# Performance work log

Hardware: AMD Instinct MI355X
Metric: run time of the kernel (lower is better)

Reference implementation:

```python
import jax, jax.numpy as jnp
import numpy as np

D_MODEL = 1024
N_HEADS = 16
D_K = D_MODEL // N_HEADS
THETA = 10000.0
MAX_SEQ_LEN = 2048


def _rope_tables(seq_len):
    pos = jnp.arange(seq_len, dtype=jnp.float32)
    inv_freq = 1.0 / (THETA ** (jnp.arange(0, D_K, 2, dtype=jnp.float32) / D_K))
    ang = pos[:, None] * inv_freq[None, :]  # [T, D_K/2]
    return jnp.cos(ang), jnp.sin(ang)


def _apply_rope(x, cos, sin):
    # x: [..., T, D_K]; cos/sin: [T, D_K/2]
    x_even = x[..., ::2]
    x_odd = x[..., 1::2]
    r_even = x_even * cos - x_odd * sin
    r_odd = x_even * sin + x_odd * cos
    out = jnp.stack([r_even, r_odd], axis=-1)  # [..., T, D_K/2, 2]
    return out.reshape(x.shape)


def setup_inputs() -> dict:
    key = jax.random.key(0)
    ks = jax.random.split(key, 5)
    std = np.sqrt(2.0 / (D_MODEL + D_MODEL))
    x = jax.random.normal(ks[0], (2, 2048, D_MODEL), dtype=jnp.float32)
    w_q = jax.random.normal(ks[1], (D_MODEL, D_MODEL), dtype=jnp.float32) * std
    w_k = jax.random.normal(ks[2], (D_MODEL, D_MODEL), dtype=jnp.float32) * std
    w_v = jax.random.normal(ks[3], (D_MODEL, D_MODEL), dtype=jnp.float32) * std
    w_o = jax.random.normal(ks[4], (D_MODEL, D_MODEL), dtype=jnp.float32) * std
    return {"x": x, "w_q": w_q, "w_k": w_k, "w_v": w_v, "w_o": w_o}


def reference(x, w_q, w_k, w_v, w_o):
    B, T, _ = x.shape
    # projections: weight stored as [d_out, d_in], y = x @ W^T
    q = jnp.einsum('btd,od->bto', x, w_q)
    k = jnp.einsum('btd,od->bto', x, w_k)
    v = jnp.einsum('btd,od->bto', x, w_v)
    # split heads: [B, T, H*Dk] -> [B, H, T, Dk]
    q = q.reshape(B, T, N_HEADS, D_K).transpose(0, 2, 1, 3)
    k = k.reshape(B, T, N_HEADS, D_K).transpose(0, 2, 1, 3)
    v = v.reshape(B, T, N_HEADS, D_K).transpose(0, 2, 1, 3)
    cos, sin = _rope_tables(T)
    q = _apply_rope(q, cos, sin)
    k = _apply_rope(k, cos, sin)
    scores = jnp.einsum('bhqd,bhkd->bhqk', q, k) / np.sqrt(D_K).astype(np.float32)
    causal = jnp.tril(jnp.ones((T, T), dtype=bool))
    scores = jnp.where(causal, scores, -jnp.inf)
    attn = jax.nn.softmax(scores, axis=-1)
    out = jnp.einsum('bhqk,bhkd->bhqd', attn, v)
    out = out.transpose(0, 2, 1, 3).reshape(B, T, D_MODEL)
    return jnp.einsum('btd,od->bto', out, w_o)
```

## Files before the change

### kernel.cpp

```cpp
#include <hip/hip_runtime.h>
#include <hip/hip_bf16.h>

typedef __bf16 bf16_t;
typedef __bf16 bf16x8 __attribute__((ext_vector_type(8)));
typedef float f32x4 __attribute__((ext_vector_type(4)));
typedef short short4v __attribute__((ext_vector_type(4)));
typedef unsigned int uint2v __attribute__((ext_vector_type(2)));

#define D_MODEL 1024
#define T_SEQ 2048
#define NH 16
#define DKD 64
#define X_ELEMS (4194304u)
#define W_ELEMS (1048576u)
#define Q_SCALE 0.18033688011112042f

__device__ __forceinline__ void async16(const bf16_t* g, bf16_t* l) {
    __builtin_amdgcn_global_load_lds((const __attribute__((address_space(1))) void*)g,
                                     (__attribute__((address_space(3))) void*)l, 16, 0, 0);
}

__device__ __forceinline__ unsigned ldsa(const bf16_t* p) {
    return (unsigned)(size_t)(const __attribute__((address_space(3))) bf16_t*)p;
}

__global__ __launch_bounds__(256) void convert_kernel(
    const float* __restrict__ x, const float* __restrict__ wq,
    const float* __restrict__ wk, const float* __restrict__ wv,
    const float* __restrict__ wo,
    bf16_t* __restrict__ xb, bf16_t* __restrict__ wqb, bf16_t* __restrict__ wkb,
    bf16_t* __restrict__ wvb, bf16_t* __restrict__ wob)
{
    size_t idx = ((size_t)blockIdx.x * 256 + threadIdx.x) * 4;
    const float* src; bf16_t* dst; size_t off;
    if (idx < X_ELEMS) { src = x; dst = xb; off = idx; }
    else {
        size_t r = idx - X_ELEMS;
        unsigned w = (unsigned)(r >> 20);
        off = r & (W_ELEMS - 1);
        src = (w == 0) ? wq : (w == 1) ? wk : (w == 2) ? wv : wo;
        dst = (w == 0) ? wqb : (w == 1) ? wkb : (w == 2) ? wvb : wob;
    }
    float4 v = *(const float4*)(src + off);
    union { bf16_t b[4]; short4v s; } u;
    u.b[0] = (bf16_t)v.x; u.b[1] = (bf16_t)v.y;
    u.b[2] = (bf16_t)v.z; u.b[3] = (bf16_t)v.w;
    *(short4v*)(dst + off) = u.s;
}

__global__ __launch_bounds__(256) void rope_kernel(float* __restrict__ cost, float* __restrict__ sint)
{
    int idx = blockIdx.x * 256 + threadIdx.x;
    int t = idx >> 5, i = idx & 31;
    float inv = expf(-0.28782313662425572f * (float)i);
    float ang = (float)t * inv;
    float s, c;
    sincosf(ang, &s, &c);
    cost[idx] = c; sint[idx] = s;
}

__global__ __launch_bounds__(256) void gemm_fused(
    const bf16_t* __restrict__ A,
    const bf16_t* __restrict__ W0, const bf16_t* __restrict__ W1, const bf16_t* __restrict__ W2,
    bf16_t* __restrict__ qout, bf16_t* __restrict__ kout, bf16_t* __restrict__ vout,
    const float* __restrict__ cost, const float* __restrict__ sint,
    float* __restrict__ fout, int modeBase)
{
    const int K = 1024;
    __shared__ bf16_t As[128 * 32];
    __shared__ bf16_t Bs[128 * 32];
    const int tid = threadIdx.x;
    const int wave = tid >> 6, lane = tid & 63;
    const int quad = lane >> 4, l16 = lane & 15;
    const int m0 = blockIdx.x * 128;
    const int n0 = blockIdx.y * 128;
    const int wm = (wave >> 1) * 64, wn = (wave & 1) * 64;
    const int mode = modeBase + blockIdx.z;
    const bf16_t* W = (mode == 1) ? W1 : (mode == 2) ? W2 : W0;

    const bf16_t* Afrag = (mode == 2) ? Bs : As;
    const bf16_t* Bfrag = (mode == 2) ? As : Bs;
    const int aoff = (mode == 2) ? wn : wm;
    const int boff = (mode == 2) ? wm : wn;

    const f32x4 fzero = {0.f, 0.f, 0.f, 0.f};
    f32x4 acc[4][4];
    #pragma unroll
    for (int i = 0; i < 4; ++i)
        #pragma unroll
        for (int j = 0; j < 4; ++j) acc[i][j] = fzero;

    for (int k0 = 0; k0 < K; k0 += 32) {
        __syncthreads();
        #pragma unroll
        for (int c = 0; c < 2; ++c) {
            int G = c * 256 + tid;
            int row = G >> 2, go = G & 3;
            async16(A + (size_t)(m0 + row) * K + (k0 + go * 8), As + (size_t)(c * 256 + wave * 64) * 8);
            async16(W + (size_t)(n0 + row) * K + (k0 + go * 8), Bs + (size_t)(c * 256 + wave * 64) * 8);
        }
        __syncthreads();
        bf16x8 af[4], bfv[4];
        #pragma unroll
        for (int mi = 0; mi < 4; ++mi)
            af[mi] = *(const bf16x8*)(Afrag + (aoff + mi * 16 + l16) * 32 + quad * 8);
        #pragma unroll
        for (int ni = 0; ni < 4; ++ni)
            bfv[ni] = *(const bf16x8*)(Bfrag + (boff + ni * 16 + l16) * 32 + quad * 8);
        #pragma unroll
        for (int mi = 0; mi < 4; ++mi)
            #pragma unroll
            for (int ni = 0; ni < 4; ++ni)
                acc[mi][ni] = __builtin_amdgcn_mfma_f32_16x16x32_bf16(af[mi], bfv[ni], acc[mi][ni], 0, 0, 0);
    }

    #pragma unroll
    for (int mi = 0; mi < 4; ++mi) {
        #pragma unroll
        for (int ni = 0; ni < 4; ++ni) {
            #pragma unroll
            for (int reg = 0; reg < 4; ++reg) {
                float v = acc[mi][ni][reg];
                if (mode == 2) {
                    int f   = n0 + wn + mi * 16 + quad * 4 + reg;
                    int tok = m0 + wm + ni * 16 + l16;
                    int t = tok & (T_SEQ - 1), b = tok >> 11;
                    int h = f >> 6, dk = f & 63;
                    vout[(((size_t)b * NH + h) * DKD + dk) * T_SEQ + t] = (bf16_t)v;
                } else {
                    int row = m0 + wm + mi * 16 + quad * 4 + reg;
                    int col = n0 + wn + ni * 16 + l16;
                    if (mode == 3) {
                        fout[(size_t)row * D_MODEL + col] = v;
                    } else {
                        int t = row & (T_SEQ - 1), b = row >> 11;
                        int h = col >> 6, dk = col & 63;
                        float vp = __shfl_xor(v, 1);
                        int fi = dk >> 1;
                        float c = cost[t * 32 + fi], s = sint[t * 32 + fi];
                        float r = (dk & 1) ? (vp * s + v * c) : (v * c - vp * s);
                        if (mode == 0) r *= Q_SCALE;
                        bf16_t* dst = (mode == 0) ? qout : kout;
                        dst[(((size_t)b * NH + h) * T_SEQ + t) * DKD + dk] = (bf16_t)r;
                    }
                }
            }
        }
    }
}

__global__ __launch_bounds__(256, 4) void attn_kernel(
    const bf16_t* __restrict__ Q, const bf16_t* __restrict__ Kb,
    const bf16_t* __restrict__ Vt, bf16_t* __restrict__ O,
    float* __restrict__ Opart, float* __restrict__ Lpart)
{
    __shared__ bf16_t Vs[2][4096];
    __shared__ bf16_t Ks[2][4096];
    const int tid = threadIdx.x;
    const int w = tid >> 6;
    const int lane = tid & 63;
    const int quad = lane >> 4, l16 = lane & 15;
    const int sig = ((quad & 1) << 1) | (quad >> 1);
    const int m7 = l16 & 15 & 7;
    const int bh = blockIdx.x;

    int v = 39 - (int)blockIdx.y;
    int g = 0, po = 0;
    for (;; ++g) {
        const int C = (g + 4) >> 2;
        if (v < C) break;
        v -= C;
        if (g >= 4) po += C;
    }
    const int c = v;
    const int ktlo = 8 * c;
    const int kthi = min(8 * c + 8, 2 * g + 2);
    const int qw = (4 * g + w) * 32;

    const bf16_t* kbase = Kb + (size_t)bh * T_SEQ * DKD;
    const bf16_t* vbase = Vt + (size_t)bh * DKD * T_SEQ;

    const int srow = tid >> 3;
    const int sgr  = (tid & 7) ^ (srow & 7);
    const bf16_t* vsrc = vbase + (size_t)srow * T_SEQ + sgr * 8;
    const bf16_t* ksrc = kbase + (size_t)srow * DKD + sgr * 8;

    const unsigned o0  = (unsigned)((l16 * 64 + ((sig ^ m7) * 8)) << 1);
    const unsigned o1  = (unsigned)((l16 * 64 + (((sig + 4) ^ m7) * 8)) << 1);
    const unsigned ko0 = (unsigned)((l16 * 64 + ((quad ^ m7) * 8)) << 1);
    const unsigned ko1 = (unsigned)((l16 * 64 + (((quad + 4) ^ m7) * 8)) << 1);
    const unsigned vb0 = ldsa(Vs[0]), vb1 = ldsa(Vs[1]);
    const unsigned kb0 = ldsa(Ks[0]), kb1 = ldsa(Ks[1]);

    bf16x8 qf[2][2];
    #pragma unroll
    for (int j = 0; j < 2; ++j) {
        const bf16_t* qp = Q + ((size_t)bh * T_SEQ + qw + j * 16 + l16) * DKD;
        qf[j][0] = *(const bf16x8*)(qp + quad * 8);
        qf[j][1] = *(const bf16x8*)(qp + 32 + quad * 8);
    }
    const f32x4 fzero = {0.f, 0.f, 0.f, 0.f};
    f32x4 oacc[2][4];
    #pragma unroll
    for (int j = 0; j < 2; ++j)
        #pragma unroll
        for (int i = 0; i < 4; ++i) oacc[j][i] = fzero;
    float lsum[2] = {0.f, 0.f};

    {
        const bf16_t* vs_ = vsrc + ktlo * 64;
        const bf16_t* ks_ = ksrc + (size_t)ktlo * 64 * DKD;
        async16(vs_,         &Vs[0][0] + w * 512);
        async16(vs_ + 65536, &Vs[0][0] + 2048 + w * 512);
        async16(ks_,         &Ks[0][0] + w * 512);
        async16(ks_ + 2048,  &Ks[0][0] + 2048 + w * 512);
    }
    asm volatile("s_waitcnt vmcnt(0)" ::: "memory");
    __syncthreads();

#define ATT_TILE(VNP, KNP, VCA, KCA) do { \
    const int k0 = kt * 64; \
    if (kt + 1 < kthi) { \
        const bf16_t* vs_ = vsrc + (k0 + 64); \
        const bf16_t* ks_ = ksrc + (size_t)(k0 + 64) * DKD; \
        async16(vs_,         (VNP) + w * 512); \
        async16(vs_ + 65536, (VNP) + 2048 + w * 512); \
        async16(ks_,         (KNP) + w * 512); \
        async16(ks_ + 2048,  (KNP) + 2048 + w * 512); \
    } \
    __builtin_amdgcn_sched_barrier(0); \
    bf16x8 kc00, kc01, kc10, kc11, kc20, kc21, kc30, kc31; \
    { const unsigned kaA = (KCA) + ko0, kaB = (KCA) + ko1; \
      asm volatile( \
        "ds_read_b128 %0, %8 offset:0\n\t" \
        "ds_read_b128 %1, %9 offset:0\n\t" \
        "ds_read_b128 %2, %8 offset:2048\n\t" \
        "ds_read_b128 %3, %9 offset:2048\n\t" \
        "ds_read_b128 %4, %8 offset:4096\n\t" \
        "ds_read_b128 %5, %9 offset:4096\n\t" \
        "ds_read_b128 %6, %8 offset:6144\n\t" \
        "ds_read_b128 %7, %9 offset:6144\n\t" \
        "s_waitcnt lgkmcnt(0)" \
        : "=&v"(kc00), "=&v"(kc01), "=&v"(kc10), "=&v"(kc11), \
          "=&v"(kc20), "=&v"(kc21), "=&v"(kc30), "=&v"(kc31) \
        : "v"(kaA), "v"(kaB)); } \
    __builtin_amdgcn_sched_barrier(0); \
    _Pragma("unroll") \
    for (int j = 0; j < 2; ++j) { \
      if (k0 <= qw + j * 16 + 15) {    \
        const int qcol = qw + j * 16 + l16; \
        f32x4 s[4]; \
        s[0] = __builtin_amdgcn_mfma_f32_16x16x32_bf16(kc00, qf[j][0], fzero, 0, 0, 0); \
        s[0] = __builtin_amdgcn_mfma_f32_16x16x32_bf16(kc01, qf[j][1], s[0], 0, 0, 0); \
        s[1] = __builtin_amdgcn_mfma_f32_16x16x32_bf16(kc10, qf[j][0], fzero, 0, 0, 0); \
        s[1] = __builtin_amdgcn_mfma_f32_16x16x32_bf16(kc11, qf[j][1], s[1], 0, 0, 0); \
        s[2] = __builtin_amdgcn_mfma_f32_16x16x32_bf16(kc20, qf[j][0], fzero, 0, 0, 0); \
        s[2] = __builtin_amdgcn_mfma_f32_16x16x32_bf16(kc21, qf[j][1], s[2], 0, 0, 0); \
        s[3] = __builtin_amdgcn_mfma_f32_16x16x32_bf16(kc30, qf[j][0], fzero, 0, 0, 0); \
        s[3] = __builtin_amdgcn_mfma_f32_16x16x32_bf16(kc31, qf[j][1], s[3], 0, 0, 0); \
        if (k0 + 63 > qw + j * 16) { \
            _Pragma("unroll") \
            for (int fi = 0; fi < 4; ++fi) \
                _Pragma("unroll") \
                for (int reg = 0; reg < 4; ++reg) { \
                    int key = k0 + fi * 16 + quad * 4 + reg; \
                    s[fi][reg] = (key > qcol) ? -__builtin_inff() : s[fi][reg]; \
                } \
        } \
        float sm = 0.f; \
        _Pragma("unroll") \
        for (int fi = 0; fi < 4; ++fi) \
            _Pragma("unroll") \
            for (int reg = 0; reg < 4; ++reg) { \
                float p = __builtin_amdgcn_exp2f(s[fi][reg]); \
                s[fi][reg] = p; sm += p; \
            } \
        lsum[j] += sm; \
        unsigned wv[4][2]; \
        _Pragma("unroll") \
        for (int fi = 0; fi < 4; ++fi) { \
            asm("v_cvt_pk_bf16_f32 %0, %1, %2" : "=v"(wv[fi][0]) : "v"(s[fi][0]), "v"(s[fi][1])); \
            asm("v_cvt_pk_bf16_f32 %0, %1, %2" : "=v"(wv[fi][1]) : "v"(s[fi][2]), "v"(s[fi][3])); \
        } \
        uint2v r0 = __builtin_amdgcn_permlane16_swap(wv[0][0], wv[1][0], false, false); \
        uint2v r1 = __builtin_amdgcn_permlane16_swap(wv[0][1], wv[1][1], false, false); \
        uint2v r2 = __builtin_amdgcn_permlane16_swap(wv[2][0], wv[3][0], false, false); \
        uint2v r3 = __builtin_amdgcn_permlane16_swap(wv[2][1], wv[3][1], false, false); \
        union { unsigned uu[4]; bf16x8 vv; } p0, p1; \
        p0.uu[0] = r0[0]; p0.uu[1] = r1[0]; p0.uu[2] = r0[1]; p0.uu[3] = r1[1]; \
        p1.uu[0] = r2[0]; p1.uu[1] = r3[0]; p1.uu[2] = r2[1]; p1.uu[3] = r3[1]; \
        const unsigned vA = (VCA) + o0, vB = (VCA) + o1; \
        bf16x8 w0a, w0b, w1a, w1b; \
        __builtin_amdgcn_sched_barrier(0); \
        asm volatile( \
            "ds_read_b128 %0, %4 offset:0\n\t" \
            "ds_read_b128 %1, %5 offset:0\n\t" \
            "ds_read_b128 %2, %4 offset:2048\n\t" \
            "ds_read_b128 %3, %5 offset:2048\n\t" \
            "s_waitcnt lgkmcnt(0)" \
            : "=&v"(w0a), "=&v"(w0b), "=&v"(w1a), "=&v"(w1b) \
            : "v"(vA), "v"(vB)); \
        __builtin_amdgcn_sched_barrier(0); \
        oacc[j][0] = __builtin_amdgcn_mfma_f32_16x16x32_bf16(w0a, p0.vv, oacc[j][0], 0, 0, 0); \
        oacc[j][0] = __builtin_amdgcn_mfma_f32_16x16x32_bf16(w0b, p1.vv, oacc[j][0], 0, 0, 0); \
        oacc[j][1] = __builtin_amdgcn_mfma_f32_16x16x32_bf16(w1a, p0.vv, oacc[j][1], 0, 0, 0); \
        oacc[j][1] = __builtin_amdgcn_mfma_f32_16x16x32_bf16(w1b, p1.vv, oacc[j][1], 0, 0, 0); \
        bf16x8 w2a, w2b, w3a, w3b; \
        asm volatile( \
            "ds_read_b128 %0, %4 offset:4096\n\t" \
            "ds_read_b128 %1, %5 offset:4096\n\t" \
            "ds_read_b128 %2, %4 offset:6144\n\t" \
            "ds_read_b128 %3, %5 offset:6144\n\t" \
            "s_waitcnt lgkmcnt(0)" \
            : "=&v"(w2a), "=&v"(w2b), "=&v"(w3a), "=&v"(w3b) \
            : "v"(vA), "v"(vB)); \
        __builtin_amdgcn_sched_barrier(0); \
        oacc[j][2] = __builtin_amdgcn_mfma_f32_16x16x32_bf16(w2a, p0.vv, oacc[j][2], 0, 0, 0); \
        oacc[j][2] = __builtin_amdgcn_mfma_f32_16x16x32_bf16(w2b, p1.vv, oacc[j][2], 0, 0, 0); \
        oacc[j][3] = __builtin_amdgcn_mfma_f32_16x16x32_bf16(w3a, p0.vv, oacc[j][3], 0, 0, 0); \
        oacc[j][3] = __builtin_amdgcn_mfma_f32_16x16x32_bf16(w3b, p1.vv, oacc[j][3], 0, 0, 0); \
      } \
    } \
    asm volatile("s_waitcnt vmcnt(0)" ::: "memory"); \
    __syncthreads(); \
} while (0)

    bool flip = false;
    for (int kt = ktlo; kt < kthi; ++kt) {
        if (!flip) { ATT_TILE(&Vs[1][0], &Ks[1][0], vb0, kb0); }
        else       { ATT_TILE(&Vs[0][0], &Ks[0][0], vb1, kb1); }
        flip = !flip;
    }
#undef ATT_TILE

    if (g < 4) {
        const int b = bh >> 4, h = bh & 15;
        #pragma unroll
        for (int j = 0; j < 2; ++j) {
            float l = lsum[j];
            l += __shfl_xor(l, 16);
            l += __shfl_xor(l, 32);
            float rl = 1.0f / l;
            int q = qw + j * 16 + l16;
            #pragma unroll
            for (int di = 0; di < 4; ++di) {
                union { bf16_t hh[4]; unsigned long long u64; } ok;
                #pragma unroll
                for (int reg = 0; reg < 4; ++reg) ok.hh[reg] = (bf16_t)(oacc[j][di][reg] * rl);
                int d = di * 16 + quad * 4;
                *(unsigned long long*)(O + ((size_t)b * T_SEQ + q) * D_MODEL + h * DKD + d) = ok.u64;
            }
        }
    } else {
        const size_t slot = (size_t)bh * 36 + po + c;
        float* op = Opart + slot * 8192 + (size_t)w * 2048;
        #pragma unroll
        for (int j = 0; j < 2; ++j) {
            Lpart[slot * 512 + w * 128 + j * 64 + lane] = lsum[j];
            #pragma unroll
            for (int di = 0; di < 4; ++di)
                *(f32x4*)(op + ((size_t)(j * 4 + di) * 64 + lane) * 4) = oacc[j][di];
        }
    }
}

__global__ __launch_bounds__(256) void combine_kernel(
    const float* __restrict__ Opart, const float* __restrict__ Lpart, bf16_t* __restrict__ O)
{
    const int bh = blockIdx.x;
    const int g = 4 + blockIdx.y;
    const int C = (g + 4) >> 2;
    int po0 = 0;
    for (int gg = 4; gg < g; ++gg) po0 += (gg + 4) >> 2;
    const int t = threadIdx.x;
    const int ql = t >> 3;
    const int d0 = (t & 7) * 8;
    const int j = ql >> 4, l16 = ql & 15;
    const int di = d0 >> 4;
    const int quad0 = (d0 & 15) >> 2;
    const int b = bh >> 4, h = bh & 15;
    const size_t sb = (size_t)bh * 36 + po0;

    for (int w = 0; w < 4; ++w) {
        float l = 0.f;
        for (int cc = 0; cc < C; ++cc) {
            const float* L = Lpart + (sb + cc) * 512 + w * 128 + j * 64 + l16;
            #pragma unroll
            for (int q = 0; q < 4; ++q) l += L[q * 16];
        }
        const float rl = 1.0f / l;
        union { bf16_t hh[8]; bf16x8 vv; } ov;
        #pragma unroll
        for (int g2 = 0; g2 < 2; ++g2) {
            const int off = ((j * 4 + di) * 64 + (quad0 + g2) * 16 + l16) * 4;
            f32x4 acc = {0.f, 0.f, 0.f, 0.f};
            for (int cc = 0; cc < C; ++cc)
                acc += *(const f32x4*)(Opart + (sb + cc) * 8192 + (size_t)w * 2048 + off);
            #pragma unroll
            for (int reg = 0; reg < 4; ++reg)
                ov.hh[g2 * 4 + reg] = (bf16_t)(acc[reg] * rl);
        }
        const int q = g * 128 + w * 32 + ql;
        *(bf16x8*)(O + ((size_t)b * T_SEQ + q) * D_MODEL + h * DKD + d0) = ov.vv;
    }
}

extern "C" void kernel_launch(void* const* d_in, const int* in_sizes, int n_in,
                              void* d_out, int out_size, void* d_ws, size_t ws_size,
                              hipStream_t stream)
{
    const float* x  = (const float*)d_in[0];
    const float* wq = (const float*)d_in[1];
    const float* wk = (const float*)d_in[2];
    const float* wv = (const float*)d_in[3];
    const float* wo = (const float*)d_in[4];
    float* out = (float*)d_out;

    char* ws = (char*)d_ws;
    size_t off = 0;
    auto alloc = [&](size_t bytes) -> void* {
        void* p = ws + off; off += (bytes + 255) & ~(size_t)255; return p;
    };
    bf16_t* xb   = (bf16_t*)alloc((size_t)X_ELEMS * 2);
    bf16_t* wqb  = (bf16_t*)alloc((size_t)W_ELEMS * 2);
    bf16_t* wkb  = (bf16_t*)alloc((size_t)W_ELEMS * 2);
    bf16_t* wvb  = (bf16_t*)alloc((size_t)W_ELEMS * 2);
    bf16_t* wob  = (bf16_t*)alloc((size_t)W_ELEMS * 2);
    bf16_t* qb   = (bf16_t*)alloc((size_t)X_ELEMS * 2);
    bf16_t* kb   = (bf16_t*)alloc((size_t)X_ELEMS * 2);
    bf16_t* vtb  = (bf16_t*)alloc((size_t)X_ELEMS * 2);
    bf16_t* ob   = (bf16_t*)alloc((size_t)X_ELEMS * 2);
    float*  cost = (float*)alloc((size_t)T_SEQ * 32 * 4);
    float*  sint = (float*)alloc((size_t)T_SEQ * 32 * 4);
    float*  opart = (float*)alloc((size_t)32 * 36 * 8192 * 4);
    float*  lpart = (float*)alloc((size_t)32 * 36 * 512 * 4);

    convert_kernel<<<8192, 256, 0, stream>>>(x, wq, wk, wv, wo, xb, wqb, wkb, wvb, wob);
    rope_kernel<<<256, 256, 0, stream>>>(cost, sint);
    gemm_fused<<<dim3(32, 8, 3), 256, 0, stream>>>(xb, wqb, wkb, wvb, qb, kb, vtb, cost, sint, nullptr, 0);
    attn_kernel<<<dim3(32, 40), 256, 0, stream>>>(qb, kb, vtb, ob, opart, lpart);
    combine_kernel<<<dim3(32, 12), 256, 0, stream>>>(opart, lpart, ob);
    gemm_fused<<<dim3(32, 8, 1), 256, 0, stream>>>(ob, wob, nullptr, nullptr, nullptr, nullptr, nullptr,
                                                   cost, sint, out, 3);
}
```

Baseline: 202.6 us.

## Split-K output projection with atomics and merge rope/zeroing into convert kernel

The output projection GEMM is split along K into two halves across blockIdx.z, and each half accumulates into the fp32 output with atomicAdd. This doubles the block count from 256 to 512 to fill more CUs. The output is zeroed and the rope tables are built inside the convert kernel, which removes one launch. In exchange the output takes an extra 16MB zeroing write, atomic traffic and a nondeterministic summation order.

```diff
diff --git a/kernel.cpp b/kernel.cpp
--- a/kernel.cpp
+++ b/kernel.cpp
@@ -29,34 +29,39 @@
     const float* __restrict__ wk, const float* __restrict__ wv,
     const float* __restrict__ wo,
     bf16_t* __restrict__ xb, bf16_t* __restrict__ wqb, bf16_t* __restrict__ wkb,
-    bf16_t* __restrict__ wvb, bf16_t* __restrict__ wob)
+    bf16_t* __restrict__ wvb, bf16_t* __restrict__ wob,
+    float* __restrict__ cost, float* __restrict__ sint, float* __restrict__ outz)
 {
-    size_t idx = ((size_t)blockIdx.x * 256 + threadIdx.x) * 4;
-    const float* src; bf16_t* dst; size_t off;
-    if (idx < X_ELEMS) { src = x; dst = xb; off = idx; }
-    else {
-        size_t r = idx - X_ELEMS;
-        unsigned w = (unsigned)(r >> 20);
-        off = r & (W_ELEMS - 1);
-        src = (w == 0) ? wq : (w == 1) ? wk : (w == 2) ? wv : wo;
-        dst = (w == 0) ? wqb : (w == 1) ? wkb : (w == 2) ? wvb : wob;
-    }
-    float4 v = *(const float4*)(src + off);
-    union { bf16_t b[4]; short4v s; } u;
-    u.b[0] = (bf16_t)v.x; u.b[1] = (bf16_t)v.y;
-    u.b[2] = (bf16_t)v.z; u.b[3] = (bf16_t)v.w;
-    *(short4v*)(dst + off) = u.s;
-}
-
-__global__ __launch_bounds__(256) void rope_kernel(float* __restrict__ cost, float* __restrict__ sint)
-{
-    int idx = blockIdx.x * 256 + threadIdx.x;
-    int t = idx >> 5, i = idx & 31;
-    float inv = expf(-0.28782313662425572f * (float)i);
-    float ang = (float)t * inv;
-    float s, c;
-    sincosf(ang, &s, &c);
-    cost[idx] = c; sint[idx] = s;
+    const unsigned bid = blockIdx.x;
+    if (bid < 8192) {
+        size_t idx = ((size_t)bid * 256 + threadIdx.x) * 4;
+        const float* src; bf16_t* dst; size_t off;
+        if (idx < X_ELEMS) { src = x; dst = xb; off = idx; }
+        else {
+            size_t r = idx - X_ELEMS;
+            unsigned w = (unsigned)(r >> 20);
+            off = r & (W_ELEMS - 1);
+            src = (w == 0) ? wq : (w == 1) ? wk : (w == 2) ? wv : wo;
+            dst = (w == 0) ? wqb : (w == 1) ? wkb : (w == 2) ? wvb : wob;
+        }
+        float4 v = *(const float4*)(src + off);
+        union { bf16_t b[4]; short4v s; } u;
+        u.b[0] = (bf16_t)v.x; u.b[1] = (bf16_t)v.y;
+        u.b[2] = (bf16_t)v.z; u.b[3] = (bf16_t)v.w;
+        *(short4v*)(dst + off) = u.s;
+    } else if (bid < 8448) {
+        int idx = (int)(bid - 8192) * 256 + threadIdx.x;
+        int t = idx >> 5, i = idx & 31;
+        float inv = expf(-0.28782313662425572f * (float)i);
+        float ang = (float)t * inv;
+        float s, c;
+        sincosf(ang, &s, &c);
+        cost[idx] = c; sint[idx] = s;
+    } else {
+        size_t idx = ((size_t)(bid - 8448) * 256 + threadIdx.x) * 4;
+        float4 z = {0.f, 0.f, 0.f, 0.f};
+        *(float4*)(outz + idx) = z;
+    }
 }
 
 __global__ __launch_bounds__(256) void gemm_fused(
@@ -83,6 +88,9 @@
     const int aoff = (mode == 2) ? wn : wm;
     const int boff = (mode == 2) ? wm : wn;
 
+    const int kLo = (mode >= 3) ? (mode - 3) * 512 : 0;
+    const int kHi = (mode >= 3) ? kLo + 512 : K;
+
     const f32x4 fzero = {0.f, 0.f, 0.f, 0.f};
     f32x4 acc[4][4];
     #pragma unroll
@@ -90,7 +98,7 @@
         #pragma unroll
         for (int j = 0; j < 4; ++j) acc[i][j] = fzero;
 
-    for (int k0 = 0; k0 < K; k0 += 32) {
+    for (int k0 = kLo; k0 < kHi; k0 += 32) {
         __syncthreads();
         #pragma unroll
         for (int c = 0; c < 2; ++c) {
@@ -130,8 +138,8 @@
                 } else {
                     int row = m0 + wm + mi * 16 + quad * 4 + reg;
                     int col = n0 + wn + ni * 16 + l16;
-                    if (mode == 3) {
-                        fout[(size_t)row * D_MODEL + col] = v;
+                    if (mode >= 3) {
+                        atomicAdd(fout + (size_t)row * D_MODEL + col, v);
                     } else {
                         int t = row & (T_SEQ - 1), b = row >> 11;
                         int h = col >> 6, dk = col & 63;
@@ -161,7 +169,7 @@
     const int lane = tid & 63;
     const int quad = lane >> 4, l16 = lane & 15;
     const int sig = ((quad & 1) << 1) | (quad >> 1);
-    const int m7 = l16 & 15 & 7;
+    const int m7 = l16 & 7;
     const int bh = blockIdx.x;
 
     int v = 39 - (int)blockIdx.y;
@@ -435,11 +443,11 @@
     float*  opart = (float*)alloc((size_t)32 * 36 * 8192 * 4);
     float*  lpart = (float*)alloc((size_t)32 * 36 * 512 * 4);
 
-    convert_kernel<<<8192, 256, 0, stream>>>(x, wq, wk, wv, wo, xb, wqb, wkb, wvb, wob);
-    rope_kernel<<<256, 256, 0, stream>>>(cost, sint);
+    convert_kernel<<<12544, 256, 0, stream>>>(x, wq, wk, wv, wo, xb, wqb, wkb, wvb, wob,
+                                              cost, sint, out);
     gemm_fused<<<dim3(32, 8, 3), 256, 0, stream>>>(xb, wqb, wkb, wvb, qb, kb, vtb, cost, sint, nullptr, 0);
     attn_kernel<<<dim3(32, 40), 256, 0, stream>>>(qb, kb, vtb, ob, opart, lpart);
     combine_kernel<<<dim3(32, 12), 256, 0, stream>>>(opart, lpart, ob);
-    gemm_fused<<<dim3(32, 8, 1), 256, 0, stream>>>(ob, wob, nullptr, nullptr, nullptr, nullptr, nullptr,
+    gemm_fused<<<dim3(32, 8, 2), 256, 0, stream>>>(ob, wob, nullptr, nullptr, nullptr, nullptr, nullptr,
                                                    cost, sint, out, 3);
 }
```

Measured after the change: 223.9 us. +10.5%, slower.
